# Kernel tuning notes

Hardware: AMD Instinct MI355X
Metric: run time of the kernel (lower is better)

## Reference

```python
import jax, jax.numpy as jnp
import numpy as np

NUM_TOKENS = 8192
CODEBOOK_DIM = 64
BETA = 0.25
DECAY = 0.99
EPS = 1e-05
B, C, H, W = 32, 64, 32, 32


def setup_inputs() -> dict:
    key = jax.random.key(0)
    k1, k2, k3, k4 = jax.random.split(key, 4)
    z = jax.random.normal(k1, (B, C, H, W), dtype=jnp.float32)
    emb = jax.random.normal(k2, (NUM_TOKENS, CODEBOOK_DIM), dtype=jnp.float32)
    ema_w = jax.random.normal(k3, (NUM_TOKENS, CODEBOOK_DIM), dtype=jnp.float32)
    cluster_size = jax.random.uniform(k4, (NUM_TOKENS,), dtype=jnp.float32)
    return {"z": z, "emb": emb, "ema_w": ema_w, "cluster_size": cluster_size}


def reference(z, emb, ema_w, cluster_size):
    # NCHW -> NHWC, flatten to [N, D]
    z_nhwc = jnp.transpose(z, (0, 2, 3, 1))
    z_flat = z_nhwc.reshape(-1, CODEBOOK_DIM)  # [N, D]

    # squared distances: ||z||^2 + ||e||^2 - 2 z e^T  -> [N, K]
    d = (jnp.sum(z_flat * z_flat, axis=1, keepdims=True)
         + jnp.sum(emb * emb, axis=1)
         - 2.0 * jnp.einsum('nd,kd->nk', z_flat, emb))
    idx = jnp.argmin(d, axis=1)  # [N] int

    z_q = emb[idx].reshape(z_nhwc.shape)  # gather + reshape

    # EMA updates (training-mode buffer math); one-hot matmuls expressed as segment sums
    new_cluster = jax.ops.segment_sum(jnp.ones_like(idx, dtype=z.dtype), idx, num_segments=NUM_TOKENS)
    cs = DECAY * cluster_size + (1.0 - DECAY) * new_cluster
    new_ema_w = jax.ops.segment_sum(z_flat, idx, num_segments=NUM_TOKENS)
    ema_w_out = DECAY * ema_w + (1.0 - DECAY) * new_ema_w
    cs_sum = jnp.sum(cs)
    cs_norm = (cs + EPS) / (cs_sum + NUM_TOKENS * EPS)
    emb_out = ema_w_out / cs_norm[:, None]

    # commitment loss uses z_q from the OLD codebook (as in torch code)
    loss = BETA * jnp.mean((jax.lax.stop_gradient(z_q) - z_nhwc) ** 2)

    # straight-through estimator, back to NCHW
    z_q_st = z_nhwc + jax.lax.stop_gradient(z_q - z_nhwc)
    z_q_st = jnp.transpose(z_q_st, (0, 3, 1, 2))
    return z_q_st, loss, idx, cs_norm, ema_w_out, emb_out
```

## Files before the change

### kernel.cpp

```cpp
#include <hip/hip_runtime.h>
#include <float.h>

#define N_TOK   32768
#define DIM     64
#define K_CODES 8192
#define HWSZ    1024
#define CHW     65536
#define NELEM   2097152

typedef short  bf16x8 __attribute__((ext_vector_type(8)));
typedef float  f32x16 __attribute__((ext_vector_type(16)));

static __device__ __forceinline__ unsigned short f2bf(float x) {
    unsigned u = __float_as_uint(x);
    unsigned r = u + 0x7FFFu + ((u >> 16) & 1u);
    return (unsigned short)(r >> 16);
}
static __device__ __forceinline__ float bf2f(unsigned short h) {
    return __uint_as_float(((unsigned)h) << 16);
}

__global__ __launch_bounds__(256) void prep_e(const float* __restrict__ emb,
                                              const float* __restrict__ ema_w,
                                              unsigned short* __restrict__ blob,
                                              float* __restrict__ eng,
                                              unsigned long long* __restrict__ packed,
                                              int* __restrict__ cnt_i,
                                              float* __restrict__ sums,
                                              float* __restrict__ emao_out) {
    __shared__ float part[512];
    const int gid = blockIdx.x * 256 + threadIdx.x;
    packed[gid] = ~0ull;
    if (gid < K_CODES) cnt_i[gid] = 0;
    if (gid < 2) sums[gid] = 0.f;

    #pragma unroll
    for (int j = 0; j < 16; ++j) {
        int i = gid + j * 32768;
        emao_out[i] = 0.99f * ema_w[i];
    }

    int tile = blockIdx.x;
    #pragma unroll
    for (int u0 = 0; u0 < 2; ++u0) {
        int u = threadIdx.x + u0 * 256;
        int s = u >> 7, h = (u >> 6) & 1, n = u & 63;
        const float* src = emb + (tile * 64 + n) * 64 + s * 16 + h * 8;
        float4 v0 = *(const float4*)src;
        float4 v1 = *(const float4*)(src + 4);
        float x[8] = {v0.x, v0.y, v0.z, v0.w, v1.x, v1.y, v1.z, v1.w};
        unsigned short hi[8], lo[8];
        float ss = 0.f;
        #pragma unroll
        for (int j = 0; j < 8; ++j) {
            hi[j] = f2bf(x[j]);
            lo[j] = f2bf(x[j] - bf2f(hi[j]));
            ss += x[j] * x[j];
        }
        part[u] = ss;
        unsigned short* dhi = blob + (size_t)tile * 8192 + ((s * 2 + 0) * 2 + h) * 512 + n * 8;
        unsigned short* dlo = blob + (size_t)tile * 8192 + ((s * 2 + 1) * 2 + h) * 512 + n * 8;
        uint4 ph, pl;
        ph.x = (unsigned)hi[0] | ((unsigned)hi[1] << 16);
        ph.y = (unsigned)hi[2] | ((unsigned)hi[3] << 16);
        ph.z = (unsigned)hi[4] | ((unsigned)hi[5] << 16);
        ph.w = (unsigned)hi[6] | ((unsigned)hi[7] << 16);
        pl.x = (unsigned)lo[0] | ((unsigned)lo[1] << 16);
        pl.y = (unsigned)lo[2] | ((unsigned)lo[3] << 16);
        pl.z = (unsigned)lo[4] | ((unsigned)lo[5] << 16);
        pl.w = (unsigned)lo[6] | ((unsigned)lo[7] << 16);
        *(uint4*)dhi = ph;
        *(uint4*)dlo = pl;
    }
    __syncthreads();
    if (threadIdx.x < 64) {
        float s = 0.f;
        #pragma unroll
        for (int j = 0; j < 8; ++j) s += part[threadIdx.x + j * 64];
        eng[tile * 64 + threadIdx.x] = s;
    }
}

__global__ __launch_bounds__(256, 3) void vq_argmin(const float* __restrict__ z,
                                                    const unsigned short* __restrict__ blob,
                                                    const float* __restrict__ eng,
                                                    unsigned long long* __restrict__ packed) {
    __shared__ __align__(16) unsigned short zh[64 * 72];
    __shared__ __align__(16) unsigned short zl[64 * 72];
    __shared__ unsigned long long red[64 * 4];

    const int tid  = threadIdx.x;
    const int lane = tid & 63;
    const int wid  = tid >> 6;
    const int l31  = lane & 31, h = lane >> 5;

    const int tb = blockIdx.x & 511;
    const int ks = blockIdx.x >> 9;
    const int n0 = tb * 64;
    const int zbase = (n0 >> 10) * CHW + (n0 & 1023);

    {
        int f4 = tid & 15;
        int c0 = tid >> 4;
        #pragma unroll
        for (int r = 0; r < 4; ++r) {
            int c = c0 * 4 + r;
            float4 v = *(const float4*)(z + zbase + c * HWSZ + f4 * 4);
            float x[4] = {v.x, v.y, v.z, v.w};
            #pragma unroll
            for (int e = 0; e < 4; ++e) {
                int t = f4 * 4 + e;
                float xs = -2.0f * x[e];
                unsigned short hi = f2bf(xs);
                zh[t * 72 + c] = hi;
                zl[t * 72 + c] = f2bf(xs - bf2f(hi));
            }
        }
    }
    __syncthreads();

    bf16x8 T0h[4], T0l[4], T1h[4], T1l[4];
    {
        int r0 = l31;
        int r1 = 32 + l31;
        #pragma unroll
        for (int s = 0; s < 4; ++s) {
            T0h[s] = *(const bf16x8*)(&zh[r0 * 72 + s * 16 + h * 8]);
            T0l[s] = *(const bf16x8*)(&zl[r0 * 72 + s * 16 + h * 8]);
            T1h[s] = *(const bf16x8*)(&zh[r1 * 72 + s * 16 + h * 8]);
            T1l[s] = *(const bf16x8*)(&zl[r1 * 72 + s * 16 + h * 8]);
        }
    }

    const int hk0 = ks * 128 + wid;
    const unsigned short* bp = blob + (size_t)(hk0 >> 1) * 8192 + ((hk0 & 1) * 32 + l31) * 8;
    const float* ep = eng + (hk0 >> 1) * 64 + (hk0 & 1) * 32 + 4 * h;
    int scode = __builtin_amdgcn_readfirstlane((hk0 >> 1) * 64 + (hk0 & 1) * 32);

    bf16x8 Eh[4], El[4];
    #pragma unroll
    for (int s = 0; s < 4; ++s) {
        Eh[s] = *(const bf16x8*)(bp + (4 * s + h) * 512);
        El[s] = *(const bf16x8*)(bp + (4 * s + 2 + h) * 512);
    }
    float4 g0 = *(const float4*)(ep);
    float4 g1 = *(const float4*)(ep + 8);
    float4 g2 = *(const float4*)(ep + 16);
    float4 g3 = *(const float4*)(ep + 24);

    float minv0 = FLT_MAX, minv1 = FLT_MAX;
    int   mini0 = 0,       mini1 = 0;

    for (int i = 0; i < 32; ++i) {
        f32x16 ac0, ac1;
        ac0[0]  = g0.x; ac0[1]  = g0.y; ac0[2]  = g0.z; ac0[3]  = g0.w;
        ac0[4]  = g1.x; ac0[5]  = g1.y; ac0[6]  = g1.z; ac0[7]  = g1.w;
        ac0[8]  = g2.x; ac0[9]  = g2.y; ac0[10] = g2.z; ac0[11] = g2.w;
        ac0[12] = g3.x; ac0[13] = g3.y; ac0[14] = g3.z; ac0[15] = g3.w;
        ac1 = ac0;

        ep += 128;
        g0 = *(const float4*)(ep);
        g1 = *(const float4*)(ep + 8);
        g2 = *(const float4*)(ep + 16);
        g3 = *(const float4*)(ep + 24);

        __builtin_amdgcn_s_setprio(1);
        #pragma unroll
        for (int s = 0; s < 4; ++s) {
            ac0 = __builtin_amdgcn_mfma_f32_32x32x16_bf16(El[s], T0h[s], ac0, 0, 0, 0);
            ac1 = __builtin_amdgcn_mfma_f32_32x32x16_bf16(El[s], T1h[s], ac1, 0, 0, 0);
            ac0 = __builtin_amdgcn_mfma_f32_32x32x16_bf16(Eh[s], T0l[s], ac0, 0, 0, 0);
            ac1 = __builtin_amdgcn_mfma_f32_32x32x16_bf16(Eh[s], T1l[s], ac1, 0, 0, 0);
            ac0 = __builtin_amdgcn_mfma_f32_32x32x16_bf16(Eh[s], T0h[s], ac0, 0, 0, 0);
            ac1 = __builtin_amdgcn_mfma_f32_32x32x16_bf16(Eh[s], T1h[s], ac1, 0, 0, 0);
        }
        __builtin_amdgcn_s_setprio(0);

        bp += 2 * 8192;
        #pragma unroll
        for (int s = 0; s < 4; ++s) {
            Eh[s] = *(const bf16x8*)(bp + (4 * s + h) * 512);
            El[s] = *(const bf16x8*)(bp + (4 * s + 2 + h) * 512);
        }

        #pragma unroll
        for (int r = 0; r < 16; ++r) {
            int code = scode + ((r & 3) + 8 * (r >> 2));
            if (ac0[r] < minv0) { minv0 = ac0[r]; mini0 = code; }
            if (ac1[r] < minv1) { minv1 = ac1[r]; mini1 = code; }
        }
        scode += 128;
    }
    mini0 += 4 * h;
    mini1 += 4 * h;

    unsigned u0 = __float_as_uint(minv0);
    u0 = (u0 & 0x80000000u) ? ~u0 : (u0 | 0x80000000u);
    unsigned long long k0 = ((unsigned long long)u0 << 32) | (unsigned)mini0;
    unsigned u1 = __float_as_uint(minv1);
    u1 = (u1 & 0x80000000u) ? ~u1 : (u1 | 0x80000000u);
    unsigned long long k1 = ((unsigned long long)u1 << 32) | (unsigned)mini1;
    unsigned long long o0 = __shfl_xor(k0, 32, 64);
    if (o0 < k0) k0 = o0;
    unsigned long long o1 = __shfl_xor(k1, 32, 64);
    if (o1 < k1) k1 = o1;
    if (h == 0) {
        red[l31 * 4 + wid]        = k0;
        red[(32 + l31) * 4 + wid] = k1;
    }
    __syncthreads();
    if (tid < 64) {
        unsigned long long a = red[tid * 4], b = red[tid * 4 + 1];
        unsigned long long c = red[tid * 4 + 2], d = red[tid * 4 + 3];
        unsigned long long m = (b < a) ? b : a;
        if (c < m) m = c;
        if (d < m) m = d;
        atomicMin(&packed[n0 + tid], m);
    }
}

__global__ __launch_bounds__(256) void zq_loss(const float* __restrict__ z,
                                               const float* __restrict__ emb,
                                               const unsigned long long* __restrict__ packed,
                                               float* __restrict__ zq_out,
                                               float* __restrict__ idx_out,
                                               int* __restrict__ idx_i32,
                                               int* __restrict__ cnt_i,
                                               float* __restrict__ loss_sum,
                                               float* __restrict__ emao_out) {
    __shared__ float e_lds[64][68];
    __shared__ float z_lds[64][68];

    const int tid = threadIdx.x;
    const int n0  = blockIdx.x * 64;
    const int t   = tid >> 2, q = tid & 3;
    const int n   = n0 + t;
    const int w   = tid >> 6, lane = tid & 63;
    const int b   = n0 >> 10;
    const int hw0 = n0 & 1023;
    const int zb  = b * CHW + hw0;

    const int idx = (int)(packed[n] & 0xFFFFFFFFull);
    if (q == 0) {
        idx_out[n] = (float)idx;
        idx_i32[n] = idx;
        atomicAdd(&cnt_i[idx], 1);
    }
    {
        const float* er = emb + idx * 64 + q * 16;
        float4 e0 = *(const float4*)er,       e1 = *(const float4*)(er + 4);
        float4 e2 = *(const float4*)(er + 8), e3 = *(const float4*)(er + 12);
        *(float4*)&e_lds[t][q * 16]      = e0;
        *(float4*)&e_lds[t][q * 16 + 4]  = e1;
        *(float4*)&e_lds[t][q * 16 + 8]  = e2;
        *(float4*)&e_lds[t][q * 16 + 12] = e3;
    }
    {
        const int f4 = tid & 15, c0 = tid >> 4;
        #pragma unroll
        for (int r = 0; r < 4; ++r) {
            int c = c0 * 4 + r;
            float4 v = *(const float4*)(z + zb + c * HWSZ + f4 * 4);
            z_lds[f4 * 4 + 0][c] = v.x;
            z_lds[f4 * 4 + 1][c] = v.y;
            z_lds[f4 * 4 + 2][c] = v.z;
            z_lds[f4 * 4 + 3][c] = v.w;
        }
    }
    __syncthreads();

    #pragma unroll
    for (int u = 0; u < 16; ++u) {
        int tt = w * 16 + u;
        int ix = __shfl(idx, u * 4, 64);
        atomicAdd(&emao_out[ix * 64 + lane], 0.01f * z_lds[tt][lane]);
    }

    {
        const int f4 = tid & 15, c0 = tid >> 4;
        #pragma unroll
        for (int r = 0; r < 4; ++r) {
            int c = c0 * 4 + r;
            float4 o;
            { float zv = z_lds[f4*4+0][c]; o.x = zv + (e_lds[f4*4+0][c] - zv); }
            { float zv = z_lds[f4*4+1][c]; o.y = zv + (e_lds[f4*4+1][c] - zv); }
            { float zv = z_lds[f4*4+2][c]; o.z = zv + (e_lds[f4*4+2][c] - zv); }
            { float zv = z_lds[f4*4+3][c]; o.w = zv + (e_lds[f4*4+3][c] - zv); }
            *(float4*)(zq_out + zb + c * HWSZ + f4 * 4) = o;
        }
    }
    float lsum = 0.f;
    #pragma unroll
    for (int j = 0; j < 16; ++j) {
        int c = q * 16 + j;
        float dd = e_lds[t][c] - z_lds[t][c];
        lsum += dd * dd;
    }
    #pragma unroll
    for (int m = 32; m >= 1; m >>= 1) lsum += __shfl_xor(lsum, m, 64);
    if ((tid & 63) == 0) atomicAdd(loss_sum, lsum);
}

__global__ __launch_bounds__(1024) void scan_cs(const int* __restrict__ cnt_i,
                                                const float* __restrict__ csize,
                                                const float* __restrict__ loss_sum,
                                                float* __restrict__ csn_out,
                                                float* __restrict__ loss_out) {
    __shared__ float sf[1024];
    const int tid = threadIdx.x;
    int v[8];
    float cv[8], fpart = 0.f;
    #pragma unroll
    for (int j = 0; j < 8; ++j) v[j] = cnt_i[tid * 8 + j];
    #pragma unroll
    for (int j = 0; j < 8; ++j) {
        cv[j] = 0.99f * csize[tid * 8 + j] + 0.01f * (float)v[j];
        fpart += cv[j];
    }
    sf[tid] = fpart;
    __syncthreads();
    for (int off = 512; off >= 1; off >>= 1) {
        if (tid < off) sf[tid] += sf[tid + off];
        __syncthreads();
    }
    float denom = sf[0] + (float)(K_CODES * 1e-5);
    #pragma unroll
    for (int j = 0; j < 8; ++j) csn_out[tid * 8 + j] = (cv[j] + 1e-5f) / denom;
    if (tid == 0) *loss_out = 0.25f * (*loss_sum) * (1.0f / (float)NELEM);
}

__global__ __launch_bounds__(256) void final_div(const float* __restrict__ emao_out,
                                                 const float* __restrict__ csn_out,
                                                 float* __restrict__ embo_out) {
    int g = blockIdx.x * 256 + threadIdx.x;
    embo_out[g] = emao_out[g] / csn_out[g >> 6];
}

extern "C" void kernel_launch(void* const* d_in, const int* in_sizes, int n_in,
                              void* d_out, int out_size, void* d_ws, size_t ws_size,
                              hipStream_t stream) {
    (void)in_sizes; (void)n_in; (void)out_size; (void)ws_size;
    const float* z     = (const float*)d_in[0];
    const float* emb   = (const float*)d_in[1];
    const float* ema_w = (const float*)d_in[2];
    const float* csize = (const float*)d_in[3];

    float* out      = (float*)d_out;
    float* zq_out   = out;
    float* loss_out = out + 2097152;
    float* idx_out  = out + 2097153;
    float* csn_out  = out + 2129921;
    float* emao_out = out + 2138113;
    float* embo_out = out + 2662401;

    char* wsb = (char*)d_ws;
    unsigned short*     blob    = (unsigned short*)(wsb);
    float*              eng     = (float*)(wsb + 2097152);
    unsigned long long* packed  = (unsigned long long*)(wsb + 2129920);
    int*                idx_i32 = (int*)(wsb + 2392064);
    int*                cnt_i   = (int*)(wsb + 2523136);
    float*              sums    = (float*)(wsb + 2555904);

    prep_e<<<128, 256, 0, stream>>>(emb, ema_w, blob, eng, packed, cnt_i, sums, emao_out);
    vq_argmin<<<1024, 256, 0, stream>>>(z, blob, eng, packed);
    zq_loss<<<N_TOK / 64, 256, 0, stream>>>(z, emb, packed, zq_out, idx_out,
                                            idx_i32, cnt_i, sums + 1, emao_out);
    scan_cs<<<1, 1024, 0, stream>>>(cnt_i, csize, sums + 1, csn_out, loss_out);
    final_div<<<K_CODES * DIM / 256, 256, 0, stream>>>(emao_out, csn_out, embo_out);
}
```

Measured before the change: 201.2 us.

## Split argmin codebook range across more blocks and fuse cluster-norm into final divide

The argmin kernel now launches twice as many blocks, each scanning half as many codebook chunks, which raises occupancy and parallelism at the cost of more atomic min merges on the packed results. The single-block scan kernel and the final divide kernel are merged into one grid-wide kernel. The cluster-size total is computed analytically as 0.99*sum(csize) + 0.01*N, with sum(csize) reduced early in prep_e. This removes one launch and the serial 1024-thread reduction, but the float summation order changes slightly.

```diff
diff --git a/kernel.cpp b/kernel.cpp
--- a/kernel.cpp
+++ b/kernel.cpp
@@ -22,6 +22,7 @@
 
 __global__ __launch_bounds__(256) void prep_e(const float* __restrict__ emb,
                                               const float* __restrict__ ema_w,
+                                              const float* __restrict__ csize,
                                               unsigned short* __restrict__ blob,
                                               float* __restrict__ eng,
                                               unsigned long long* __restrict__ packed,
@@ -29,15 +30,27 @@
                                               float* __restrict__ sums,
                                               float* __restrict__ emao_out) {
     __shared__ float part[512];
+    __shared__ float csp[4];
     const int gid = blockIdx.x * 256 + threadIdx.x;
     packed[gid] = ~0ull;
     if (gid < K_CODES) cnt_i[gid] = 0;
-    if (gid < 2) sums[gid] = 0.f;
+    if (gid == 1) sums[1] = 0.f;
 
     #pragma unroll
     for (int j = 0; j < 16; ++j) {
         int i = gid + j * 32768;
         emao_out[i] = 0.99f * ema_w[i];
+    }
+
+    if (blockIdx.x == 0) {
+        float s = 0.f;
+        #pragma unroll
+        for (int j = 0; j < 32; ++j) s += csize[threadIdx.x * 32 + j];
+        #pragma unroll
+        for (int m = 32; m >= 1; m >>= 1) s += __shfl_xor(s, m, 64);
+        if ((threadIdx.x & 63) == 0) csp[threadIdx.x >> 6] = s;
+        __syncthreads();
+        if (threadIdx.x == 0) sums[0] = csp[0] + csp[1] + csp[2] + csp[3];
     }
 
     int tile = blockIdx.x;
@@ -132,7 +145,7 @@
         }
     }
 
-    const int hk0 = ks * 128 + wid;
+    const int hk0 = ks * 64 + wid;
     const unsigned short* bp = blob + (size_t)(hk0 >> 1) * 8192 + ((hk0 & 1) * 32 + l31) * 8;
     const float* ep = eng + (hk0 >> 1) * 64 + (hk0 & 1) * 32 + 4 * h;
     int scode = __builtin_amdgcn_readfirstlane((hk0 >> 1) * 64 + (hk0 & 1) * 32);
@@ -151,7 +164,7 @@
     float minv0 = FLT_MAX, minv1 = FLT_MAX;
     int   mini0 = 0,       mini1 = 0;
 
-    for (int i = 0; i < 32; ++i) {
+    for (int i = 0; i < 16; ++i) {
         f32x16 ac0, ac1;
         ac0[0]  = g0.x; ac0[1]  = g0.y; ac0[2]  = g0.z; ac0[3]  = g0.w;
         ac0[4]  = g1.x; ac0[5]  = g1.y; ac0[6]  = g1.z; ac0[7]  = g1.w;
@@ -302,39 +315,21 @@
     if ((tid & 63) == 0) atomicAdd(loss_sum, lsum);
 }
 
-__global__ __launch_bounds__(1024) void scan_cs(const int* __restrict__ cnt_i,
+__global__ __launch_bounds__(256) void norm_div(const int* __restrict__ cnt_i,
                                                 const float* __restrict__ csize,
-                                                const float* __restrict__ loss_sum,
+                                                const float* __restrict__ sums,
+                                                const float* __restrict__ emao_out,
                                                 float* __restrict__ csn_out,
-                                                float* __restrict__ loss_out) {
-    __shared__ float sf[1024];
-    const int tid = threadIdx.x;
-    int v[8];
-    float cv[8], fpart = 0.f;
-    #pragma unroll
-    for (int j = 0; j < 8; ++j) v[j] = cnt_i[tid * 8 + j];
-    #pragma unroll
-    for (int j = 0; j < 8; ++j) {
-        cv[j] = 0.99f * csize[tid * 8 + j] + 0.01f * (float)v[j];
-        fpart += cv[j];
-    }
-    sf[tid] = fpart;
-    __syncthreads();
-    for (int off = 512; off >= 1; off >>= 1) {
-        if (tid < off) sf[tid] += sf[tid + off];
-        __syncthreads();
-    }
-    float denom = sf[0] + (float)(K_CODES * 1e-5);
-    #pragma unroll
-    for (int j = 0; j < 8; ++j) csn_out[tid * 8 + j] = (cv[j] + 1e-5f) / denom;
-    if (tid == 0) *loss_out = 0.25f * (*loss_sum) * (1.0f / (float)NELEM);
-}
-
-__global__ __launch_bounds__(256) void final_div(const float* __restrict__ emao_out,
-                                                 const float* __restrict__ csn_out,
-                                                 float* __restrict__ embo_out) {
-    int g = blockIdx.x * 256 + threadIdx.x;
-    embo_out[g] = emao_out[g] / csn_out[g >> 6];
+                                                float* __restrict__ loss_out,
+                                                float* __restrict__ embo_out) {
+    const int g = blockIdx.x * 256 + threadIdx.x;
+    const int c = g >> 6;
+    const float denom = 0.99f * sums[0] + 0.01f * (float)N_TOK + (float)(K_CODES * 1e-5);
+    const float cv  = 0.99f * csize[c] + 0.01f * (float)cnt_i[c];
+    const float csn = (cv + 1e-5f) / denom;
+    if ((g & 63) == 0) csn_out[c] = csn;
+    embo_out[g] = emao_out[g] / csn;
+    if (g == 0) *loss_out = 0.25f * sums[1] * (1.0f / (float)NELEM);
 }
 
 extern "C" void kernel_launch(void* const* d_in, const int* in_sizes, int n_in,
@@ -362,10 +357,11 @@
     int*                cnt_i   = (int*)(wsb + 2523136);
     float*              sums    = (float*)(wsb + 2555904);
 
-    prep_e<<<128, 256, 0, stream>>>(emb, ema_w, blob, eng, packed, cnt_i, sums, emao_out);
-    vq_argmin<<<1024, 256, 0, stream>>>(z, blob, eng, packed);
+    prep_e<<<128, 256, 0, stream>>>(emb, ema_w, csize, blob, eng, packed, cnt_i,
+                                    sums, emao_out);
+    vq_argmin<<<2048, 256, 0, stream>>>(z, blob, eng, packed);
     zq_loss<<<N_TOK / 64, 256, 0, stream>>>(z, emb, packed, zq_out, idx_out,
                                             idx_i32, cnt_i, sums + 1, emao_out);
-    scan_cs<<<1, 1024, 0, stream>>>(cnt_i, csize, sums + 1, csn_out, loss_out);
-    final_div<<<K_CODES * DIM / 256, 256, 0, stream>>>(emao_out, csn_out, embo_out);
-}
+    norm_div<<<NELEM / 4 / 256, 256, 0, stream>>>(cnt_i, csize, sums, emao_out,
+                                                  csn_out, loss_out, embo_out);
+}
```

Measured after the change: 204.9 us. Within noise of the previous version (+1.8%).
